# Performance work log

Hardware: AMD Instinct MI355X
Metric: run time of the kernel (lower is better)

The kernel has to match this reference:

```python
import jax, jax.numpy as jnp
import numpy as np

EMBED_DIM = 1024
NUM_HEADS = 16
HEAD_DIM = EMBED_DIM // NUM_HEADS


def _sinusoid_pos_emb(seq_len, dim):
    pos = jnp.arange(seq_len, dtype=jnp.float32)
    idx = jnp.arange(dim // 2, dtype=jnp.float32)
    inv_freq = 1.0 / (10000.0 ** (2.0 * idx / dim))
    ang = pos[:, None] * inv_freq[None, :]          # [S, D/2]
    return jnp.concatenate([jnp.sin(ang), jnp.cos(ang)], axis=-1)  # [S, D]


def _relative_shift(x):
    # x: [B, H, S, S] -> Transformer-XL shift
    b, h, s, _ = x.shape
    x = jnp.pad(x, ((0, 0), (0, 0), (0, 0), (1, 0)))
    x = x.reshape(b, h, s + 1, s)
    return x[:, :, 1:, :].reshape(b, h, s, s)


def setup_inputs() -> dict:
    key = jax.random.key(0)
    ks = jax.random.split(key, 12)
    D = EMBED_DIM
    sc = 1.0 / np.sqrt(D)
    inp = {"x": jax.random.normal(ks[0], (2, 2048, D), dtype=jnp.float32)}
    for i, name in enumerate(["Wq", "Wk", "Wv", "Wp", "Wo"]):
        inp[name] = jax.random.normal(ks[1 + i], (D, D), dtype=jnp.float32) * sc
        inp["b" + name[1].lower()] = jnp.zeros((D,), dtype=jnp.float32)
    inp["u"] = jax.random.normal(ks[6], (1, NUM_HEADS, 1, HEAD_DIM), dtype=jnp.float32) * 0.05
    inp["v"] = jax.random.normal(ks[7], (1, NUM_HEADS, 1, HEAD_DIM), dtype=jnp.float32) * 0.05
    return inp


def reference(x, Wq, bq, Wk, bk, Wv, bv, Wp, bp, Wo, bo, u, v):
    B, S, D = x.shape
    H, P = NUM_HEADS, HEAD_DIM

    def heads(t):  # [B,S,D] -> [B,H,S,P]
        return t.reshape(B, S, H, P).transpose(0, 2, 1, 3)

    q = heads(x @ Wq + bq)
    k = heads(x @ Wk + bk)
    val = heads(x @ Wv + bv)

    pos = _sinusoid_pos_emb(S, D) @ Wp + bp            # [S, D]
    pos = pos.reshape(S, H, P).transpose(1, 0, 2)       # [H, S, P]

    content_score = jnp.einsum('bhsp,bhtp->bhst', q + u, k)
    pos_score = jnp.einsum('bhsp,htp->bhst', q + v, pos)
    pos_score = _relative_shift(pos_score)

    score = (content_score + pos_score) / jnp.sqrt(jnp.float32(P))
    weights = jax.nn.softmax(score, axis=-1)            # dropout = 0 (inference)
    out = jnp.einsum('bhst,bhtp->bhsp', weights, val)
    out = out.transpose(0, 2, 1, 3).reshape(B, S, D)
    return out @ Wo + bo
```

## Files before the change

### kernel.cpp

```cpp
#include <hip/hip_runtime.h>
#include <hip/hip_bf16.h>

typedef unsigned short u16;
typedef unsigned int u32;
typedef __bf16 bf16x8 __attribute__((ext_vector_type(8)));
typedef float f32x4 __attribute__((ext_vector_type(4)));

#define SEQ 2048
#define NH 16
#define PD 64
#define DM 1024

#if __has_builtin(__builtin_amdgcn_exp2f)
#define EXP2(x) __builtin_amdgcn_exp2f(x)
#else
#define EXP2(x) __expf((x) * 0.6931471805599453f)
#endif

__device__ __forceinline__ float bf2f(u16 s) {
  u32 t = ((u32)s) << 16;
  float f;
  __builtin_memcpy(&f, &t, 4);
  return f;
}
__device__ __forceinline__ u16 f2bf(float f) {
  u32 x;
  __builtin_memcpy(&x, &f, 4);
  x = (x + 0x7fffu + ((x >> 16) & 1u)) >> 16;
  return (u16)x;
}
__device__ __forceinline__ float u2f(u32 b) {
  float f;
  __builtin_memcpy(&f, &b, 4);
  return f;
}
__device__ __forceinline__ u32 pack2(float a, float b) {
  __hip_bfloat162 h = __float22bfloat162_rn(float2{a, b});
  u32 r;
  __builtin_memcpy(&r, &h, 4);
  return r;
}
template <int C>
__device__ __forceinline__ float dppf(float x) {
  int xi;
  __builtin_memcpy(&xi, &x, 4);
  int yi = __builtin_amdgcn_mov_dpp(xi, C, 0xF, 0xF, false);
  float y;
  __builtin_memcpy(&y, &yi, 4);
  return y;
}
__device__ __forceinline__ float rmax16(float x) {
  x = fmaxf(x, dppf<0x121>(x));
  x = fmaxf(x, dppf<0x122>(x));
  x = fmaxf(x, dppf<0x124>(x));
  x = fmaxf(x, dppf<0x128>(x));
  return x;
}
__device__ __forceinline__ float rsum16(float x) {
  x += dppf<0x121>(x);
  x += dppf<0x122>(x);
  x += dppf<0x124>(x);
  x += dppf<0x128>(x);
  return x;
}
__device__ __forceinline__ void gld16(const u16* g, u16* l) {
  __builtin_amdgcn_global_load_lds(
      (const __attribute__((address_space(1))) unsigned int*)(g),
      (__attribute__((address_space(3))) unsigned int*)(l), 16, 0, 0);
}

__global__ __launch_bounds__(256) void detect_kernel(const u16* __restrict__ probe,
                                                     int* __restrict__ flag) {
  __shared__ int sz[256], sh[256];
  int tid = threadIdx.x;
  int zeros = 0, huge = 0;
  for (int j = 0; j < 16; ++j) {
    int i = tid * 16 + j;
    u16 v = probe[i];
    int e = (v >> 7) & 0xFF;
    if (((i & 1) == 0) && v == 0) zeros++;
    if (e >= 0x8C) huge++;
  }
  sz[tid] = zeros; sh[tid] = huge;
  __syncthreads();
  for (int s = 128; s > 0; s >>= 1) {
    if (tid < s) { sz[tid] += sz[tid + s]; sh[tid] += sh[tid + s]; }
    __syncthreads();
  }
  if (tid == 0) *flag = (sz[0] > 1024 || sh[0] > 200) ? 1 : 0;
}

__global__ __launch_bounds__(256) void convert_x_kernel(const void* __restrict__ src,
                                                        u16* __restrict__ dst,
                                                        const int* __restrict__ flag) {
  int i = (blockIdx.x * 256 + threadIdx.x) * 4;
  if (*flag) {
    float4 f = *(const float4*)((const float*)src + i);
    u16 o[4] = {f2bf(f.x), f2bf(f.y), f2bf(f.z), f2bf(f.w)};
    *(uint2*)(dst + i) = *(const uint2*)o;
  } else {
    *(uint2*)(dst + i) = *(const uint2*)((const u16*)src + i);
  }
}

struct ParamPtrs { const void* p[7]; };
__global__ __launch_bounds__(256) void convert_params_kernel(ParamPtrs pp,
                                                             float* __restrict__ pf,
                                                             const int* __restrict__ flag) {
  int idx = blockIdx.x * 256 + threadIdx.x;
  int seg = idx >> 10, off = idx & 1023;
  const void* s = pp.p[seg];
  pf[idx] = (*flag) ? ((const float*)s)[off] : bf2f(((const u16*)s)[off]);
}

__global__ __launch_bounds__(256) void sinusoid_kernel(u16* __restrict__ out) {
  int idx = blockIdx.x * 256 + threadIdx.x;
  int s = idx >> 10;
  int i = idx & 1023;
  int j = i & 511;
  float invf = __expf(-(float)j * (9.210340371976184f / 512.0f));
  float ang = (float)s * invf;
  float val = (i < 512) ? sinf(ang) : cosf(ang);
  out[idx] = f2bf(val);
}

__global__ __launch_bounds__(256) void transpose5_kernel(
    const void* __restrict__ w0, const void* __restrict__ w1,
    const void* __restrict__ w2, const void* __restrict__ w3,
    const void* __restrict__ w4, u16* __restrict__ dst,
    const int* __restrict__ flag) {
  __shared__ u16 t[64][72];
  int z = blockIdx.z;
  const void* src = (z == 0) ? w0 : (z == 1) ? w1 : (z == 2) ? w2 : (z == 3) ? w3 : w4;
  u16* out = dst + (size_t)z * DM * DM;
  int r0 = blockIdx.y * 64, c0 = blockIdx.x * 64;
  int tr = threadIdx.x >> 2;
  int tc = (threadIdx.x & 3) * 16;
  if (*flag) {
    const float* g = (const float*)src + (size_t)(r0 + tr) * DM + c0 + tc;
#pragma unroll
    for (int q = 0; q < 4; ++q) {
      float4 f = *(const float4*)(g + q * 4);
      t[tr][tc + q * 4 + 0] = f2bf(f.x);
      t[tr][tc + q * 4 + 1] = f2bf(f.y);
      t[tr][tc + q * 4 + 2] = f2bf(f.z);
      t[tr][tc + q * 4 + 3] = f2bf(f.w);
    }
  } else {
    const uint4* g = (const uint4*)((const u16*)src + (size_t)(r0 + tr) * DM + c0 + tc);
    uint4 a = g[0], bb = g[1];
    *(uint4*)&t[tr][tc] = a;
    *(uint4*)&t[tr][tc + 8] = bb;
  }
  __syncthreads();
  u16 tmp[16] __attribute__((aligned(16)));
#pragma unroll
  for (int jj = 0; jj < 16; ++jj) tmp[jj] = t[tc + jj][tr];
  uint4* o = (uint4*)(out + (size_t)(c0 + tr) * DM + r0 + tc);
  o[0] = *(const uint4*)&tmp[0];
  o[1] = *(const uint4*)&tmp[8];
}

__global__ __launch_bounds__(256) void transpose_v_kernel(
    const u16* __restrict__ V, u16* __restrict__ Vt) {
  __shared__ u16 t[64][72];
  int s0 = blockIdx.x * 64;
  int bh = blockIdx.y;
  int b = bh >> 4, h = bh & 15;
  int tr = threadIdx.x >> 2;
  int tc = (threadIdx.x & 3) * 16;
  const uint4* g = (const uint4*)(V + ((size_t)(b * SEQ + s0 + tr) * NH + h) * PD + tc);
  uint4 a = g[0], bb = g[1];
  *(uint4*)&t[tr][tc] = a;
  *(uint4*)&t[tr][tc + 8] = bb;
  __syncthreads();
  u16 tmp[16] __attribute__((aligned(16)));
#pragma unroll
  for (int jj = 0; jj < 16; ++jj) tmp[jj] = t[tc + jj][tr];
  uint4* o = (uint4*)(Vt + ((size_t)(b * NH + h) * PD + tr) * SEQ + s0 + tc);
  o[0] = *(const uint4*)&tmp[0];
  o[1] = *(const uint4*)&tmp[8];
}

struct GemmArgs {
  const u16* A;  const u16* A3;
  const u16* Bt0; const u16* Bt1; const u16* Bt2; const u16* Bt3;
  const float* b0; const float* b1; const float* b2; const float* b3;
  void* C0; void* C1; void* C2; void* C3;
  int N, K, M3;
  const int* flag; int outFp32;
};

__global__ __launch_bounds__(256, 4) void gemm_bt_kernel(GemmArgs p) {
  __shared__ u16 As[128 * 32];
  __shared__ u16 Bs[128 * 32];
  int z = blockIdx.z;
  if (z == 3 && (int)blockIdx.y * 128 >= p.M3) return;
  const u16* A = (z == 3) ? p.A3 : p.A;
  const u16* Bt = (z == 0) ? p.Bt0 : (z == 1) ? p.Bt1 : (z == 2) ? p.Bt2 : p.Bt3;
  const float* bias = (z == 0) ? p.b0 : (z == 1) ? p.b1 : (z == 2) ? p.b2 : p.b3;
  void* Cv = (z == 0) ? p.C0 : (z == 1) ? p.C1 : (z == 2) ? p.C2 : p.C3;
  int K = p.K, N = p.N;
  bool f32o = p.outFp32 && (*p.flag);

  int tid = threadIdx.x;
  int wave = tid >> 6, lane = tid & 63;
  int quad = lane >> 4, l16 = lane & 15;
  int m0 = blockIdx.y * 128, n0 = blockIdx.x * 128;
  int wm = (wave >> 1) * 64, wn = (wave & 1) * 64;

  int trow = tid >> 2;
  int tcol = ((tid & 3) ^ ((tid >> 3) & 3)) * 8;
  const u16* ga = A + (size_t)(m0 + trow) * K + tcol;
  const u16* gb = Bt + (size_t)(n0 + trow) * K + tcol;
  u16* lwa = As + wave * 512;
  u16* lwb = Bs + wave * 512;
  int slotx = (quad ^ ((l16 >> 1) & 3)) * 8;

  f32x4 acc[4][4] = {};

  for (int k0 = 0; k0 < K; k0 += 32) {
    __syncthreads();
    gld16(ga + k0, lwa);
    gld16(ga + (size_t)64 * K + k0, lwa + 2048);
    gld16(gb + k0, lwb);
    gld16(gb + (size_t)64 * K + k0, lwb + 2048);
    __syncthreads();
    bf16x8 af[4], bfv[4];
#pragma unroll
    for (int i = 0; i < 4; ++i) {
      af[i] = *(const bf16x8*)&As[(wm + i * 16 + l16) * 32 + slotx];
      bfv[i] = *(const bf16x8*)&Bs[(wn + i * 16 + l16) * 32 + slotx];
    }
#pragma unroll
    for (int tm = 0; tm < 4; ++tm)
#pragma unroll
      for (int tn = 0; tn < 4; ++tn)
        acc[tm][tn] = __builtin_amdgcn_mfma_f32_16x16x32_bf16(af[tm], bfv[tn], acc[tm][tn], 0, 0, 0);
  }

#pragma unroll
  for (int tm = 0; tm < 4; ++tm) {
    int row = m0 + wm + tm * 16 + quad * 4;
#pragma unroll
    for (int tn = 0; tn < 4; ++tn) {
      int col = n0 + wn + tn * 16 + l16;
      float bv = bias[col];
#pragma unroll
      for (int r = 0; r < 4; ++r) {
        float val = acc[tm][tn][r] + bv;
        if (f32o) ((float*)Cv)[(size_t)(row + r) * N + col] = val;
        else ((u16*)Cv)[(size_t)(row + r) * N + col] = f2bf(val);
      }
    }
  }
}

__global__ __launch_bounds__(256, 4) void attn_kernel(
    const u16* __restrict__ Q, const u16* __restrict__ Kg,
    const u16* __restrict__ Vtg, const u16* __restrict__ Rg,
    const float* __restrict__ pf,
    u16* __restrict__ O) {
  __shared__ __align__(16) u16 KP[64 * 72];
  __shared__ __align__(16) u16 RVs[4096];
  __shared__ __align__(16) u16 Bb[128 * 66];

  int tid = threadIdx.x, wave = tid >> 6, lane = tid & 63;
  int quad = lane >> 4, l16 = lane & 15;
  int id = blockIdx.x;
  int bh = (id & 7) + ((id >> 8) << 3);
  int s0 = ((id >> 3) & 31) * 64;
  int b = bh >> 4, h = bh & 15;
  const float* pu = pf + 5 * 1024 + h * PD;
  const float* pv = pf + 6 * 1024 + h * PD;

  int arow = wave * 16 + l16;
  int sl_base = wave * 16 + quad * 4;

  int srow = wave * 16 + (lane >> 2);
  int scol = ((lane & 3) ^ ((lane >> 3) & 3)) * 8;
  u16* kbase = KP + wave * 512;
  u16* rvbase = RVs + wave * 512;
  int kb0 = l16 * 32 + (quad ^ ((l16 >> 1) & 3)) * 8;

  const float QS = 0.18033688011112042f;
  bf16x8 qu0, qu1, qv0a, qv1a, qv0b, qv1b;
  {
    const u16* qp = Q + ((size_t)(b * SEQ + s0 + arow)) * DM + h * PD;
    int row2 = s0 + arow + 1;
    if (row2 > SEQ - 1) row2 = SEQ - 1;
    const u16* qp2 = Q + ((size_t)(b * SEQ + row2)) * DM + h * PD;
    u16 qa[16] __attribute__((aligned(16)));
    u16 qb[16] __attribute__((aligned(16)));
    *(uint4*)&qa[0] = *(const uint4*)(qp + quad * 8);
    *(uint4*)&qa[8] = *(const uint4*)(qp + 32 + quad * 8);
    *(uint4*)&qb[0] = *(const uint4*)(qp2 + quad * 8);
    *(uint4*)&qb[8] = *(const uint4*)(qp2 + 32 + quad * 8);
    u16 fu[16] __attribute__((aligned(16)));
    u16 fv0[16] __attribute__((aligned(16)));
    u16 fv1[16] __attribute__((aligned(16)));
#pragma unroll
    for (int j = 0; j < 8; ++j) {
      float u0 = pu[quad * 8 + j], u1 = pu[32 + quad * 8 + j];
      float v0 = pv[quad * 8 + j], v1 = pv[32 + quad * 8 + j];
      fu[j] = f2bf((bf2f(qa[j]) + u0) * QS);
      fu[8 + j] = f2bf((bf2f(qa[8 + j]) + u1) * QS);
      fv0[j] = f2bf((bf2f(qa[j]) + v0) * QS);
      fv0[8 + j] = f2bf((bf2f(qa[8 + j]) + v1) * QS);
      fv1[j] = f2bf((bf2f(qb[j]) + v0) * QS);
      fv1[8 + j] = f2bf((bf2f(qb[8 + j]) + v1) * QS);
    }
    __builtin_memcpy(&qu0, &fu[0], 16);
    __builtin_memcpy(&qu1, &fu[8], 16);
    __builtin_memcpy(&qv0a, &fv0[0], 16);
    __builtin_memcpy(&qv1a, &fv0[8], 16);
    __builtin_memcpy(&qv0b, &fv1[0], 16);
    __builtin_memcpy(&qv1b, &fv1[8], 16);
  }

  auto dmaR = [&](int tb0) {
    int tg = tb0 + srow;
    tg = tg < 0 ? 0 : (tg > SEQ - 1 ? SEQ - 1 : tg);
    const u16* gr = Rg + (size_t)tg * DM + h * PD + scol;
    gld16(gr, rvbase);
    gld16(gr + 32, rvbase + 2048);
  };
  auto slice = [&](bf16x8 fa0, bf16x8 fa1, int slotBase, int rowOff, int lo, int hi) {
#pragma unroll
    for (int tt = 0; tt < 4; ++tt) {
      f32x4 pacc = {};
      bf16x8 b0 = *(const bf16x8*)&RVs[kb0 + tt * 512];
      bf16x8 b1 = *(const bf16x8*)&RVs[kb0 + tt * 512 + 2048];
      pacc = __builtin_amdgcn_mfma_f32_16x16x32_bf16(fa0, b0, pacc, 0, 0, 0);
      pacc = __builtin_amdgcn_mfma_f32_16x16x32_bf16(fa1, b1, pacc, 0, 0, 0);
      int rloc = tt * 16 + l16;
      bool ok = (rloc >= lo) & (rloc <= hi);
      u32 w0 = ok ? pack2(pacc[0], pacc[1]) : 0u;
      u32 w1 = ok ? pack2(pacc[2], pacc[3]) : 0u;
      int prow = (slotBase + rloc + rowOff) & 127;
      *(u32*)&Bb[prow * 66 + sl_base] = w0;
      *(u32*)&Bb[prow * 66 + sl_base + 2] = w1;
    }
  };

  float m_i[4], l_i[4];
#pragma unroll
  for (int r = 0; r < 4; ++r) { m_i[r] = -1e30f; l_i[r] = 0.f; }
  f32x4 oacc[4] = {};

  dmaR(SEQ - 65 - s0);
  __syncthreads();
  slice(qv0a, qv1a, 0, 0, 0, 63);

  for (int j0 = 0; j0 < SEQ; j0 += 64) {
    int a1 = (j0 >> 6) + 1;
    int slot = (a1 & 1) << 6;
    bool p0n = (j0 <= s0);
    bool p1n = (j0 >= s0);
    __syncthreads();
    {
      const u16* gk = Kg + (size_t)(b * SEQ + j0 + srow) * DM + h * PD + scol;
      gld16(gk, kbase);
      gld16(gk + 32, kbase + 2048);
    }
    dmaR((p0n ? (SEQ - 65 - s0) : (-65 - s0)) + 64 * a1);
    __syncthreads();

    f32x4 acc[4];
#pragma unroll
    for (int tn = 0; tn < 4; ++tn) {
      f32x4 a = {};
      bf16x8 b0 = *(const bf16x8*)&KP[kb0 + tn * 512];
      bf16x8 b1 = *(const bf16x8*)&KP[kb0 + tn * 512 + 2048];
      a = __builtin_amdgcn_mfma_f32_16x16x32_bf16(qu0, b0, a, 0, 0, 0);
      a = __builtin_amdgcn_mfma_f32_16x16x32_bf16(qu1, b1, a, 0, 0, 0);
      acc[tn] = a;
    }

    if (p0n) slice(qv0a, qv1a, slot, 0, 0, s0 + 64 - 64 * a1);
    if (p0n && p1n) {
      __syncthreads();
      dmaR(64 * a1 - s0 - 65);
      __syncthreads();
    }
    if (p1n) slice(qv0b, qv1b, slot, 1, s0 + 65 - 64 * a1, 63);
    __syncthreads();

    {
      const u16* gv = Vtg + ((size_t)(b * NH + h) * PD + srow) * SEQ + j0 + scol;
      gld16(gv, rvbase);
      gld16(gv + 32, rvbase + 2048);
    }

    int g0 = l16 - sl_base + 64 + j0;
#pragma unroll
    for (int tn = 0; tn < 4; ++tn) {
#pragma unroll
      for (int r = 0; r < 4; ++r) {
        int rl = (g0 + tn * 16 - r) & 127;
        acc[tn][r] += bf2f(Bb[rl * 66 + sl_base + r]);
      }
    }

    float alpha_r[4];
#pragma unroll
    for (int r = 0; r < 4; ++r) {
      float v0 = acc[0][r], v1 = acc[1][r];
      float v2 = acc[2][r], v3 = acc[3][r];
      float mx = fmaxf(fmaxf(v0, v1), fmaxf(v2, v3));
      mx = rmax16(mx);
      float m_new = fmaxf(m_i[r], mx);
      float al = EXP2(m_i[r] - m_new);
      u32 w0 = pack2(EXP2(v0 - m_new), EXP2(v1 - m_new));
      u32 w1 = pack2(EXP2(v2 - m_new), EXP2(v3 - m_new));
      u16 ec[4] = {(u16)w0, (u16)(w0 >> 16), (u16)w1, (u16)(w1 >> 16)};
      int row = sl_base + r;
      u16* prow_ = KP + row * 72 + l16;
#pragma unroll
      for (int cr = 0; cr < 4; ++cr) {
        int c = (cr + quad) & 3;
        prow_[c * 16] = ec[c];
      }
      float ssum = u2f(w0 << 16) + u2f(w0 & 0xffff0000u) + u2f(w1 << 16) + u2f(w1 & 0xffff0000u);
      ssum = rsum16(ssum);
      l_i[r] = l_i[r] * al + ssum;
      m_i[r] = m_new;
      alpha_r[r] = al;
    }
    __syncthreads();

    {
      bf16x8 pa0 = *(const bf16x8*)&KP[arow * 72 + quad * 8];
      bf16x8 pa1 = *(const bf16x8*)&KP[arow * 72 + 32 + quad * 8];
#pragma unroll
      for (int tp = 0; tp < 4; ++tp) {
#pragma unroll
        for (int r = 0; r < 4; ++r) oacc[tp][r] *= alpha_r[r];
        bf16x8 b0 = *(const bf16x8*)&RVs[kb0 + tp * 512];
        bf16x8 b1 = *(const bf16x8*)&RVs[kb0 + tp * 512 + 2048];
        oacc[tp] = __builtin_amdgcn_mfma_f32_16x16x32_bf16(pa0, b0, oacc[tp], 0, 0, 0);
        oacc[tp] = __builtin_amdgcn_mfma_f32_16x16x32_bf16(pa1, b1, oacc[tp], 0, 0, 0);
      }
    }
  }

#pragma unroll
  for (int r = 0; r < 4; ++r) l_i[r] = 1.f / l_i[r];
#pragma unroll
  for (int tp = 0; tp < 4; ++tp) {
    int pcol = tp * 16 + l16;
#pragma unroll
    for (int r = 0; r < 4; ++r) {
      int sg = s0 + sl_base + r;
      O[((size_t)(b * SEQ + sg)) * DM + h * PD + pcol] = f2bf(oacc[tp][r] * l_i[r]);
    }
  }
}

extern "C" void kernel_launch(void* const* d_in, const int* in_sizes, int n_in,
                              void* d_out, int out_size, void* d_ws, size_t ws_size,
                              hipStream_t stream) {
  (void)in_sizes; (void)n_in; (void)out_size; (void)ws_size;
  const void* x  = d_in[0];
  const void* Wq = d_in[1];
  const void* bq = d_in[2];
  const void* Wk = d_in[3];
  const void* bk = d_in[4];
  const void* Wv = d_in[5];
  const void* bv = d_in[6];
  const void* Wp = d_in[7];
  const void* bp = d_in[8];
  const void* Wo = d_in[9];
  const void* bo = d_in[10];
  const void* u  = d_in[11];
  const void* v  = d_in[12];

  char* base = (char*)d_ws;
  int* flag = (int*)base;
  float* pf = (float*)(base + 64);
  u16* wbase = (u16*)(base + 64 + 7168 * 4);
  u16* WT   = wbase;
  u16* xb   = WT + (size_t)5 * DM * DM;
  u16* sinb = xb + (size_t)2 * SEQ * DM;
  u16* Qb   = sinb + (size_t)SEQ * DM;
  u16* Kb   = Qb + (size_t)2 * SEQ * DM;
  u16* Vb   = Kb + (size_t)2 * SEQ * DM;
  u16* Rb   = Vb + (size_t)2 * SEQ * DM;
  u16* Vtb  = xb;
  u16* Ab   = Vb;

  detect_kernel<<<1, 256, 0, stream>>>((const u16*)Wq, flag);

  convert_x_kernel<<<(2 * SEQ * DM) / 1024, 256, 0, stream>>>(x, xb, flag);
  ParamPtrs pp;
  pp.p[0] = bq; pp.p[1] = bk; pp.p[2] = bv; pp.p[3] = bp; pp.p[4] = bo;
  pp.p[5] = u;  pp.p[6] = v;
  convert_params_kernel<<<28, 256, 0, stream>>>(pp, pf, flag);

  sinusoid_kernel<<<(SEQ * DM) / 256, 256, 0, stream>>>(sinb);
  transpose5_kernel<<<dim3(16, 16, 5), 256, 0, stream>>>(Wq, Wk, Wv, Wp, Wo, WT, flag);

  GemmArgs qkv;
  qkv.A = xb; qkv.A3 = sinb;
  qkv.Bt0 = WT; qkv.Bt1 = WT + (size_t)DM * DM; qkv.Bt2 = WT + (size_t)2 * DM * DM;
  qkv.Bt3 = WT + (size_t)3 * DM * DM;
  qkv.b0 = pf; qkv.b1 = pf + 1024; qkv.b2 = pf + 2048; qkv.b3 = pf + 3072;
  qkv.C0 = Qb; qkv.C1 = Kb; qkv.C2 = Vb; qkv.C3 = Rb;
  qkv.N = DM; qkv.K = DM; qkv.M3 = SEQ; qkv.flag = flag; qkv.outFp32 = 0;
  gemm_bt_kernel<<<dim3(8, 32, 4), 256, 0, stream>>>(qkv);

  transpose_v_kernel<<<dim3(32, 32), 256, 0, stream>>>(Vb, Vtb);
  attn_kernel<<<dim3(1024), 256, 0, stream>>>(Qb, Kb, Vtb, Rb, pf, Ab);

  GemmArgs fo;
  fo.A = Ab; fo.A3 = Ab;
  fo.Bt0 = WT + (size_t)4 * DM * DM; fo.Bt1 = fo.Bt0; fo.Bt2 = fo.Bt0; fo.Bt3 = fo.Bt0;
  fo.b0 = pf + 4096; fo.b1 = fo.b0; fo.b2 = fo.b0; fo.b3 = fo.b0;
  fo.C0 = d_out; fo.C1 = d_out; fo.C2 = d_out; fo.C3 = d_out;
  fo.N = DM; fo.K = DM; fo.M3 = 0; fo.flag = flag; fo.outFp32 = 1;
  gemm_bt_kernel<<<dim3(8, 32, 1), 256, 0, stream>>>(fo);
}
```

Measured before the change: 313.0 us.

## Transpose QK MFMA operands so softmax rows live per lane, restructure rel-shift buffer

Swaps the A/B operands of the score and positional MFMAs so each lane holds four consecutive key columns of one query row. Row max and sum then need only two cross-lane shuffles instead of four DPP steps per register, and one max/exp chain per lane instead of four. The relative-shift buffer becomes row-major per query (B2) with wraparound duplicate entries and precomputed even/odd offsets, and the loop is unrolled by two. Alpha and l are redistributed to the PV output layout via ds_bpermute. Separately, the sinusoid kernel switches to fast __sinf/__cosf, which costs some accuracy for large angles.

Measured after the change: 372.5 us. 19.0% more time.

```diff
diff --git a/kernel.cpp b/kernel.cpp
--- a/kernel.cpp
+++ b/kernel.cpp
@@ -29,39 +29,22 @@
   x = (x + 0x7fffu + ((x >> 16) & 1u)) >> 16;
   return (u16)x;
 }
-__device__ __forceinline__ float u2f(u32 b) {
-  float f;
-  __builtin_memcpy(&f, &b, 4);
-  return f;
-}
 __device__ __forceinline__ u32 pack2(float a, float b) {
   __hip_bfloat162 h = __float22bfloat162_rn(float2{a, b});
   u32 r;
   __builtin_memcpy(&r, &h, 4);
   return r;
 }
-template <int C>
-__device__ __forceinline__ float dppf(float x) {
+__device__ __forceinline__ float sxor(float x, int m) {
+  return __shfl_xor(x, m, 64);
+}
+__device__ __forceinline__ float bpermf(float x, int idx) {
   int xi;
   __builtin_memcpy(&xi, &x, 4);
-  int yi = __builtin_amdgcn_mov_dpp(xi, C, 0xF, 0xF, false);
+  int yi = __builtin_amdgcn_ds_bpermute(idx, xi);
   float y;
   __builtin_memcpy(&y, &yi, 4);
   return y;
-}
-__device__ __forceinline__ float rmax16(float x) {
-  x = fmaxf(x, dppf<0x121>(x));
-  x = fmaxf(x, dppf<0x122>(x));
-  x = fmaxf(x, dppf<0x124>(x));
-  x = fmaxf(x, dppf<0x128>(x));
-  return x;
-}
-__device__ __forceinline__ float rsum16(float x) {
-  x += dppf<0x121>(x);
-  x += dppf<0x122>(x);
-  x += dppf<0x124>(x);
-  x += dppf<0x128>(x);
-  return x;
 }
 __device__ __forceinline__ void gld16(const u16* g, u16* l) {
   __builtin_amdgcn_global_load_lds(
@@ -120,7 +103,7 @@
   int j = i & 511;
   float invf = __expf(-(float)j * (9.210340371976184f / 512.0f));
   float ang = (float)s * invf;
-  float val = (i < 512) ? sinf(ang) : cosf(ang);
+  float val = (i < 512) ? __sinf(ang) : __cosf(ang);
   out[idx] = f2bf(val);
 }
 
@@ -263,7 +246,7 @@
     u16* __restrict__ O) {
   __shared__ __align__(16) u16 KP[64 * 72];
   __shared__ __align__(16) u16 RVs[4096];
-  __shared__ __align__(16) u16 Bb[128 * 66];
+  __shared__ __align__(16) u16 B2[64 * 132];
 
   int tid = threadIdx.x, wave = tid >> 6, lane = tid & 63;
   int quad = lane >> 4, l16 = lane & 15;
@@ -318,6 +301,18 @@
     __builtin_memcpy(&qv1b, &fv1[8], 16);
   }
 
+  u16* B2c = B2 + (16 * wave + l16) * 132;
+  int pE[4], pO[4];
+#pragma unroll
+  for (int tn = 0; tn < 4; ++tn) {
+    pE[tn] = (16 * tn + 4 * quad + 64 - 16 * wave - l16) & 127;
+    pO[tn] = (16 * tn + 4 * quad + 128 - 16 * wave - l16) & 127;
+  }
+  int bpi[4];
+#pragma unroll
+  for (int r = 0; r < 4; ++r) bpi[r] = (20 * quad + r) * 4;
+  u16* prowP = KP + (size_t)arow * 72 + 4 * quad;
+
   auto dmaR = [&](int tb0) {
     int tg = tb0 + srow;
     tg = tg < 0 ? 0 : (tg > SEQ - 1 ? SEQ - 1 : tg);
@@ -325,36 +320,62 @@
     gld16(gr, rvbase);
     gld16(gr + 32, rvbase + 2048);
   };
-  auto slice = [&](bf16x8 fa0, bf16x8 fa1, int slotBase, int rowOff, int lo, int hi) {
+  auto slice0 = [&](bf16x8 fa0, bf16x8 fa1, int baseRow, int hi) {
 #pragma unroll
     for (int tt = 0; tt < 4; ++tt) {
       f32x4 pacc = {};
       bf16x8 b0 = *(const bf16x8*)&RVs[kb0 + tt * 512];
       bf16x8 b1 = *(const bf16x8*)&RVs[kb0 + tt * 512 + 2048];
-      pacc = __builtin_amdgcn_mfma_f32_16x16x32_bf16(fa0, b0, pacc, 0, 0, 0);
-      pacc = __builtin_amdgcn_mfma_f32_16x16x32_bf16(fa1, b1, pacc, 0, 0, 0);
-      int rloc = tt * 16 + l16;
-      bool ok = (rloc >= lo) & (rloc <= hi);
-      u32 w0 = ok ? pack2(pacc[0], pacc[1]) : 0u;
-      u32 w1 = ok ? pack2(pacc[2], pacc[3]) : 0u;
-      int prow = (slotBase + rloc + rowOff) & 127;
-      *(u32*)&Bb[prow * 66 + sl_base] = w0;
-      *(u32*)&Bb[prow * 66 + sl_base + 2] = w1;
+      pacc = __builtin_amdgcn_mfma_f32_16x16x32_bf16(b0, fa0, pacc, 0, 0, 0);
+      pacc = __builtin_amdgcn_mfma_f32_16x16x32_bf16(b1, fa1, pacc, 0, 0, 0);
+      int r0 = tt * 16 + 4 * quad;
+      float v0 = (r0 + 0 <= hi) ? pacc[0] : 0.f;
+      float v1 = (r0 + 1 <= hi) ? pacc[1] : 0.f;
+      float v2 = (r0 + 2 <= hi) ? pacc[2] : 0.f;
+      float v3 = (r0 + 3 <= hi) ? pacc[3] : 0.f;
+      uint2 w;
+      w.x = pack2(v0, v1);
+      w.y = pack2(v2, v3);
+      int u0 = (baseRow + r0) & 127;
+      *(uint2*)&B2c[u0] = w;
+      if (u0 == 0) *(uint2*)&B2c[128] = w;
     }
   };
-
-  float m_i[4], l_i[4];
-#pragma unroll
-  for (int r = 0; r < 4; ++r) { m_i[r] = -1e30f; l_i[r] = 0.f; }
+  auto slice1 = [&](bf16x8 fa0, bf16x8 fa1, int baseRow, int lo) {
+#pragma unroll
+    for (int tt = 0; tt < 4; ++tt) {
+      f32x4 pacc = {};
+      bf16x8 b0 = *(const bf16x8*)&RVs[kb0 + tt * 512];
+      bf16x8 b1 = *(const bf16x8*)&RVs[kb0 + tt * 512 + 2048];
+      pacc = __builtin_amdgcn_mfma_f32_16x16x32_bf16(b0, fa0, pacc, 0, 0, 0);
+      pacc = __builtin_amdgcn_mfma_f32_16x16x32_bf16(b1, fa1, pacc, 0, 0, 0);
+      int r0 = tt * 16 + 4 * quad;
+      float v0 = (r0 + 0 >= lo) ? pacc[0] : 0.f;
+      float v1 = (r0 + 1 >= lo) ? pacc[1] : 0.f;
+      float v2 = (r0 + 2 >= lo) ? pacc[2] : 0.f;
+      float v3 = (r0 + 3 >= lo) ? pacc[3] : 0.f;
+      u32 w0 = pack2(v0, v1), w1 = pack2(v2, v3);
+      u16 ev[4] = {(u16)w0, (u16)(w0 >> 16), (u16)w1, (u16)(w1 >> 16)};
+      int u0 = (baseRow + r0) & 127;
+#pragma unroll
+      for (int reg = 0; reg < 4; ++reg) {
+        int uu = u0 + reg;
+        B2c[uu] = ev[reg];
+        if ((uu & 127) < 3) B2c[uu ^ 128] = ev[reg];
+      }
+    }
+  };
+
+  float m_s = -1e30f, l_s = 0.f;
   f32x4 oacc[4] = {};
 
   dmaR(SEQ - 65 - s0);
   __syncthreads();
-  slice(qv0a, qv1a, 0, 0, 0, 63);
-
-  for (int j0 = 0; j0 < SEQ; j0 += 64) {
+  slice0(qv0a, qv1a, 0, 63);
+
+  auto body = [&](int j0, const int* gp) {
     int a1 = (j0 >> 6) + 1;
-    int slot = (a1 & 1) << 6;
+    int slotBase = (a1 & 1) << 6;
     bool p0n = (j0 <= s0);
     bool p1n = (j0 >= s0);
     __syncthreads();
@@ -370,20 +391,20 @@
 #pragma unroll
     for (int tn = 0; tn < 4; ++tn) {
       f32x4 a = {};
-      bf16x8 b0 = *(const bf16x8*)&KP[kb0 + tn * 512];
-      bf16x8 b1 = *(const bf16x8*)&KP[kb0 + tn * 512 + 2048];
-      a = __builtin_amdgcn_mfma_f32_16x16x32_bf16(qu0, b0, a, 0, 0, 0);
-      a = __builtin_amdgcn_mfma_f32_16x16x32_bf16(qu1, b1, a, 0, 0, 0);
+      bf16x8 k0 = *(const bf16x8*)&KP[kb0 + tn * 512];
+      bf16x8 k1 = *(const bf16x8*)&KP[kb0 + tn * 512 + 2048];
+      a = __builtin_amdgcn_mfma_f32_16x16x32_bf16(k0, qu0, a, 0, 0, 0);
+      a = __builtin_amdgcn_mfma_f32_16x16x32_bf16(k1, qu1, a, 0, 0, 0);
       acc[tn] = a;
     }
 
-    if (p0n) slice(qv0a, qv1a, slot, 0, 0, s0 + 64 - 64 * a1);
+    if (p0n) slice0(qv0a, qv1a, slotBase, s0 + 64 - 64 * a1);
     if (p0n && p1n) {
       __syncthreads();
       dmaR(64 * a1 - s0 - 65);
       __syncthreads();
     }
-    if (p1n) slice(qv0b, qv1b, slot, 1, s0 + 65 - 64 * a1, 63);
+    if (p1n) slice1(qv0b, qv1b, slotBase + 1, s0 + 65 - 64 * a1);
     __syncthreads();
 
     {
@@ -392,41 +413,44 @@
       gld16(gv + 32, rvbase + 2048);
     }
 
-    int g0 = l16 - sl_base + 64 + j0;
 #pragma unroll
     for (int tn = 0; tn < 4; ++tn) {
-#pragma unroll
-      for (int r = 0; r < 4; ++r) {
-        int rl = (g0 + tn * 16 - r) & 127;
-        acc[tn][r] += bf2f(Bb[rl * 66 + sl_base + r]);
-      }
-    }
-
+      const u16* g = B2c + gp[tn];
+      acc[tn][0] += bf2f(g[0]);
+      acc[tn][1] += bf2f(g[1]);
+      acc[tn][2] += bf2f(g[2]);
+      acc[tn][3] += bf2f(g[3]);
+    }
+
+    float t0 = fmaxf(fmaxf(acc[0][0], acc[0][1]), fmaxf(acc[0][2], acc[0][3]));
+    float t1 = fmaxf(fmaxf(acc[1][0], acc[1][1]), fmaxf(acc[1][2], acc[1][3]));
+    float t2 = fmaxf(fmaxf(acc[2][0], acc[2][1]), fmaxf(acc[2][2], acc[2][3]));
+    float t3 = fmaxf(fmaxf(acc[3][0], acc[3][1]), fmaxf(acc[3][2], acc[3][3]));
+    float mx = fmaxf(fmaxf(t0, t1), fmaxf(t2, t3));
+    mx = fmaxf(mx, sxor(mx, 16));
+    mx = fmaxf(mx, sxor(mx, 32));
+    float m_new = fmaxf(m_s, mx);
+    float al = EXP2(m_s - m_new);
+    m_s = m_new;
+    float ssum = 0.f;
+#pragma unroll
+    for (int tn = 0; tn < 4; ++tn) {
+      float e0 = EXP2(acc[tn][0] - m_new);
+      float e1 = EXP2(acc[tn][1] - m_new);
+      float e2 = EXP2(acc[tn][2] - m_new);
+      float e3 = EXP2(acc[tn][3] - m_new);
+      ssum += (e0 + e1) + (e2 + e3);
+      uint2 w;
+      w.x = pack2(e0, e1);
+      w.y = pack2(e2, e3);
+      *(uint2*)(prowP + tn * 16) = w;
+    }
+    ssum += sxor(ssum, 16);
+    ssum += sxor(ssum, 32);
+    l_s = l_s * al + ssum;
     float alpha_r[4];
 #pragma unroll
-    for (int r = 0; r < 4; ++r) {
-      float v0 = acc[0][r], v1 = acc[1][r];
-      float v2 = acc[2][r], v3 = acc[3][r];
-      float mx = fmaxf(fmaxf(v0, v1), fmaxf(v2, v3));
-      mx = rmax16(mx);
-      float m_new = fmaxf(m_i[r], mx);
-      float al = EXP2(m_i[r] - m_new);
-      u32 w0 = pack2(EXP2(v0 - m_new), EXP2(v1 - m_new));
-      u32 w1 = pack2(EXP2(v2 - m_new), EXP2(v3 - m_new));
-      u16 ec[4] = {(u16)w0, (u16)(w0 >> 16), (u16)w1, (u16)(w1 >> 16)};
-      int row = sl_base + r;
-      u16* prow_ = KP + row * 72 + l16;
-#pragma unroll
-      for (int cr = 0; cr < 4; ++cr) {
-        int c = (cr + quad) & 3;
-        prow_[c * 16] = ec[c];
-      }
-      float ssum = u2f(w0 << 16) + u2f(w0 & 0xffff0000u) + u2f(w1 << 16) + u2f(w1 & 0xffff0000u);
-      ssum = rsum16(ssum);
-      l_i[r] = l_i[r] * al + ssum;
-      m_i[r] = m_new;
-      alpha_r[r] = al;
-    }
+    for (int r = 0; r < 4; ++r) alpha_r[r] = bpermf(al, bpi[r]);
     __syncthreads();
 
     {
@@ -442,17 +466,23 @@
         oacc[tp] = __builtin_amdgcn_mfma_f32_16x16x32_bf16(pa1, b1, oacc[tp], 0, 0, 0);
       }
     }
-  }
-
-#pragma unroll
-  for (int r = 0; r < 4; ++r) l_i[r] = 1.f / l_i[r];
+  };
+
+  for (int j00 = 0; j00 < SEQ; j00 += 128) {
+    body(j00, pE);
+    body(j00 + 64, pO);
+  }
+
+  float linv[4];
+#pragma unroll
+  for (int r = 0; r < 4; ++r) linv[r] = 1.f / bpermf(l_s, bpi[r]);
 #pragma unroll
   for (int tp = 0; tp < 4; ++tp) {
     int pcol = tp * 16 + l16;
 #pragma unroll
     for (int r = 0; r < 4; ++r) {
       int sg = s0 + sl_base + r;
-      O[((size_t)(b * SEQ + sg)) * DM + h * PD + pcol] = f2bf(oacc[tp][r] * l_i[r]);
+      O[((size_t)(b * SEQ + sg)) * DM + h * PD + pcol] = f2bf(oacc[tp][r] * linv[r]);
     }
   }
 }
```

## Fuse prep kernels into one launch and write V transposed from QKV GEMM

Applied to the files above, without the earlier changes.

Merges the dtype-detect, x conversion, sinusoid generation, weight transposes and parameter conversion into a single prep kernel in which every block recomputes the detection flag itself. The separate V-transpose kernel is dropped: the QKV GEMM epilogue writes V directly in [b, h*d, s] layout with packed 4-element stores. The sinusoid now uses the fast __sinf/__cosf intrinsics. This removes several launches and a full read/write pass over V, at the cost of every prep block re-reading the probe, plus lower sin/cos accuracy for large angles.

New measurement: 302.2 us. -3.4%, faster.

```diff
diff --git a/kernel.cpp b/kernel.cpp
--- a/kernel.cpp
+++ b/kernel.cpp
@@ -69,117 +69,108 @@
       (__attribute__((address_space(3))) unsigned int*)(l), 16, 0, 0);
 }
 
-__global__ __launch_bounds__(256) void detect_kernel(const u16* __restrict__ probe,
-                                                     int* __restrict__ flag) {
+struct PrepArgs {
+  const void* x;
+  const void* w0; const void* w1; const void* w2; const void* w3; const void* w4;
+  const void* p0; const void* p1; const void* p2; const void* p3; const void* p4;
+  const void* p5; const void* p6;
+};
+
+__global__ __launch_bounds__(256) void prep_kernel(PrepArgs pa,
+                                                   u16* __restrict__ xb,
+                                                   u16* __restrict__ sinb,
+                                                   u16* __restrict__ WT,
+                                                   float* __restrict__ pf,
+                                                   int* __restrict__ flag) {
   __shared__ int sz[256], sh[256];
+  __shared__ u16 t[64][72];
   int tid = threadIdx.x;
-  int zeros = 0, huge = 0;
-  for (int j = 0; j < 16; ++j) {
-    int i = tid * 16 + j;
-    u16 v = probe[i];
-    int e = (v >> 7) & 0xFF;
-    if (((i & 1) == 0) && v == 0) zeros++;
-    if (e >= 0x8C) huge++;
-  }
-  sz[tid] = zeros; sh[tid] = huge;
-  __syncthreads();
-  for (int s = 128; s > 0; s >>= 1) {
-    if (tid < s) { sz[tid] += sz[tid + s]; sh[tid] += sh[tid + s]; }
-    __syncthreads();
-  }
-  if (tid == 0) *flag = (sz[0] > 1024 || sh[0] > 200) ? 1 : 0;
-}
-
-__global__ __launch_bounds__(256) void convert_x_kernel(const void* __restrict__ src,
-                                                        u16* __restrict__ dst,
-                                                        const int* __restrict__ flag) {
-  int i = (blockIdx.x * 256 + threadIdx.x) * 4;
-  if (*flag) {
-    float4 f = *(const float4*)((const float*)src + i);
-    u16 o[4] = {f2bf(f.x), f2bf(f.y), f2bf(f.z), f2bf(f.w)};
-    *(uint2*)(dst + i) = *(const uint2*)o;
+
+  {
+    const u16* probe = (const u16*)pa.w0;
+    int zeros = 0, huge = 0;
+    for (int j = 0; j < 16; ++j) {
+      int i = tid * 16 + j;
+      u16 v = probe[i];
+      int e = (v >> 7) & 0xFF;
+      if (((i & 1) == 0) && v == 0) zeros++;
+      if (e >= 0x8C) huge++;
+    }
+    sz[tid] = zeros; sh[tid] = huge;
+    __syncthreads();
+    for (int s = 128; s > 0; s >>= 1) {
+      if (tid < s) { sz[tid] += sz[tid + s]; sh[tid] += sh[tid + s]; }
+      __syncthreads();
+    }
+  }
+  int f = (sz[0] > 1024 || sh[0] > 200) ? 1 : 0;
+  int id = blockIdx.x;
+  if (id == 0 && tid == 0) *flag = f;
+
+  if (id < 4096) {
+    int i = (id * 256 + tid) * 4;
+    if (f) {
+      float4 fv = *(const float4*)((const float*)pa.x + i);
+      u16 o[4] __attribute__((aligned(8))) = {f2bf(fv.x), f2bf(fv.y), f2bf(fv.z), f2bf(fv.w)};
+      *(uint2*)(xb + i) = *(const uint2*)o;
+    } else {
+      *(uint2*)(xb + i) = *(const uint2*)((const u16*)pa.x + i);
+    }
+  } else if (id < 6144) {
+    int base = ((id - 4096) * 256 + tid) * 4;
+    u16 o[4] __attribute__((aligned(8)));
+#pragma unroll
+    for (int e = 0; e < 4; ++e) {
+      int idx = base + e;
+      int s = idx >> 10;
+      int i = idx & 1023;
+      int j = i & 511;
+      float invf = __expf(-(float)j * (9.210340371976184f / 512.0f));
+      float ang = (float)s * invf;
+      float val = (i < 512) ? __sinf(ang) : __cosf(ang);
+      o[e] = f2bf(val);
+    }
+    *(uint2*)(sinb + base) = *(const uint2*)o;
+  } else if (id < 7424) {
+    int tt = id - 6144;
+    int z = tt >> 8;
+    int rem = tt & 255;
+    const void* src = (z == 0) ? pa.w0 : (z == 1) ? pa.w1 : (z == 2) ? pa.w2
+                     : (z == 3) ? pa.w3 : pa.w4;
+    u16* out = WT + (size_t)z * DM * DM;
+    int r0 = (rem >> 4) * 64, c0 = (rem & 15) * 64;
+    int tr = tid >> 2;
+    int tc = (tid & 3) * 16;
+    if (f) {
+      const float* g = (const float*)src + (size_t)(r0 + tr) * DM + c0 + tc;
+#pragma unroll
+      for (int q = 0; q < 4; ++q) {
+        float4 fv = *(const float4*)(g + q * 4);
+        t[tr][tc + q * 4 + 0] = f2bf(fv.x);
+        t[tr][tc + q * 4 + 1] = f2bf(fv.y);
+        t[tr][tc + q * 4 + 2] = f2bf(fv.z);
+        t[tr][tc + q * 4 + 3] = f2bf(fv.w);
+      }
+    } else {
+      const uint4* g = (const uint4*)((const u16*)src + (size_t)(r0 + tr) * DM + c0 + tc);
+      uint4 a = g[0], bb = g[1];
+      *(uint4*)&t[tr][tc] = a;
+      *(uint4*)&t[tr][tc + 8] = bb;
+    }
+    __syncthreads();
+    u16 tmp[16] __attribute__((aligned(16)));
+#pragma unroll
+    for (int jj = 0; jj < 16; ++jj) tmp[jj] = t[tc + jj][tr];
+    uint4* o = (uint4*)(out + (size_t)(c0 + tr) * DM + r0 + tc);
+    o[0] = *(const uint4*)&tmp[0];
+    o[1] = *(const uint4*)&tmp[8];
   } else {
-    *(uint2*)(dst + i) = *(const uint2*)((const u16*)src + i);
-  }
-}
-
-struct ParamPtrs { const void* p[7]; };
-__global__ __launch_bounds__(256) void convert_params_kernel(ParamPtrs pp,
-                                                             float* __restrict__ pf,
-                                                             const int* __restrict__ flag) {
-  int idx = blockIdx.x * 256 + threadIdx.x;
-  int seg = idx >> 10, off = idx & 1023;
-  const void* s = pp.p[seg];
-  pf[idx] = (*flag) ? ((const float*)s)[off] : bf2f(((const u16*)s)[off]);
-}
-
-__global__ __launch_bounds__(256) void sinusoid_kernel(u16* __restrict__ out) {
-  int idx = blockIdx.x * 256 + threadIdx.x;
-  int s = idx >> 10;
-  int i = idx & 1023;
-  int j = i & 511;
-  float invf = __expf(-(float)j * (9.210340371976184f / 512.0f));
-  float ang = (float)s * invf;
-  float val = (i < 512) ? sinf(ang) : cosf(ang);
-  out[idx] = f2bf(val);
-}
-
-__global__ __launch_bounds__(256) void transpose5_kernel(
-    const void* __restrict__ w0, const void* __restrict__ w1,
-    const void* __restrict__ w2, const void* __restrict__ w3,
-    const void* __restrict__ w4, u16* __restrict__ dst,
-    const int* __restrict__ flag) {
-  __shared__ u16 t[64][72];
-  int z = blockIdx.z;
-  const void* src = (z == 0) ? w0 : (z == 1) ? w1 : (z == 2) ? w2 : (z == 3) ? w3 : w4;
-  u16* out = dst + (size_t)z * DM * DM;
-  int r0 = blockIdx.y * 64, c0 = blockIdx.x * 64;
-  int tr = threadIdx.x >> 2;
-  int tc = (threadIdx.x & 3) * 16;
-  if (*flag) {
-    const float* g = (const float*)src + (size_t)(r0 + tr) * DM + c0 + tc;
-#pragma unroll
-    for (int q = 0; q < 4; ++q) {
-      float4 f = *(const float4*)(g + q * 4);
-      t[tr][tc + q * 4 + 0] = f2bf(f.x);
-      t[tr][tc + q * 4 + 1] = f2bf(f.y);
-      t[tr][tc + q * 4 + 2] = f2bf(f.z);
-      t[tr][tc + q * 4 + 3] = f2bf(f.w);
-    }
-  } else {
-    const uint4* g = (const uint4*)((const u16*)src + (size_t)(r0 + tr) * DM + c0 + tc);
-    uint4 a = g[0], bb = g[1];
-    *(uint4*)&t[tr][tc] = a;
-    *(uint4*)&t[tr][tc + 8] = bb;
-  }
-  __syncthreads();
-  u16 tmp[16] __attribute__((aligned(16)));
-#pragma unroll
-  for (int jj = 0; jj < 16; ++jj) tmp[jj] = t[tc + jj][tr];
-  uint4* o = (uint4*)(out + (size_t)(c0 + tr) * DM + r0 + tc);
-  o[0] = *(const uint4*)&tmp[0];
-  o[1] = *(const uint4*)&tmp[8];
-}
-
-__global__ __launch_bounds__(256) void transpose_v_kernel(
-    const u16* __restrict__ V, u16* __restrict__ Vt) {
-  __shared__ u16 t[64][72];
-  int s0 = blockIdx.x * 64;
-  int bh = blockIdx.y;
-  int b = bh >> 4, h = bh & 15;
-  int tr = threadIdx.x >> 2;
-  int tc = (threadIdx.x & 3) * 16;
-  const uint4* g = (const uint4*)(V + ((size_t)(b * SEQ + s0 + tr) * NH + h) * PD + tc);
-  uint4 a = g[0], bb = g[1];
-  *(uint4*)&t[tr][tc] = a;
-  *(uint4*)&t[tr][tc + 8] = bb;
-  __syncthreads();
-  u16 tmp[16] __attribute__((aligned(16)));
-#pragma unroll
-  for (int jj = 0; jj < 16; ++jj) tmp[jj] = t[tc + jj][tr];
-  uint4* o = (uint4*)(Vt + ((size_t)(b * NH + h) * PD + tr) * SEQ + s0 + tc);
-  o[0] = *(const uint4*)&tmp[0];
-  o[1] = *(const uint4*)&tmp[8];
+    int idx = (id - 7424) * 256 + tid;
+    int seg = idx >> 10, off = idx & 1023;
+    const void* s = (seg == 0) ? pa.p0 : (seg == 1) ? pa.p1 : (seg == 2) ? pa.p2
+                   : (seg == 3) ? pa.p3 : (seg == 4) ? pa.p4 : (seg == 5) ? pa.p5 : pa.p6;
+    pf[idx] = f ? ((const float*)s)[off] : bf2f(((const u16*)s)[off]);
+  }
 }
 
 struct GemmArgs {
@@ -188,7 +179,7 @@
   const float* b0; const float* b1; const float* b2; const float* b3;
   void* C0; void* C1; void* C2; void* C3;
   int N, K, M3;
-  const int* flag; int outFp32;
+  const int* flag; int outFp32; int vtrans;
 };
 
 __global__ __launch_bounds__(256, 4) void gemm_bt_kernel(GemmArgs p) {
@@ -202,6 +193,7 @@
   void* Cv = (z == 0) ? p.C0 : (z == 1) ? p.C1 : (z == 2) ? p.C2 : p.C3;
   int K = p.K, N = p.N;
   bool f32o = p.outFp32 && (*p.flag);
+  bool vt = p.vtrans && (z == 2);
 
   int tid = threadIdx.x;
   int wave = tid >> 6, lane = tid & 63;
@@ -246,11 +238,19 @@
     for (int tn = 0; tn < 4; ++tn) {
       int col = n0 + wn + tn * 16 + l16;
       float bv = bias[col];
-#pragma unroll
-      for (int r = 0; r < 4; ++r) {
-        float val = acc[tm][tn][r] + bv;
-        if (f32o) ((float*)Cv)[(size_t)(row + r) * N + col] = val;
-        else ((u16*)Cv)[(size_t)(row + r) * N + col] = f2bf(val);
+      if (vt) {
+        u16 o4[4] __attribute__((aligned(8)));
+#pragma unroll
+        for (int r = 0; r < 4; ++r) o4[r] = f2bf(acc[tm][tn][r] + bv);
+        int bq_ = row >> 11, s = row & 2047;
+        *(uint2*)((u16*)Cv + ((size_t)(bq_ * 1024 + col)) * 2048 + s) = *(const uint2*)o4;
+      } else {
+#pragma unroll
+        for (int r = 0; r < 4; ++r) {
+          float val = acc[tm][tn][r] + bv;
+          if (f32o) ((float*)Cv)[(size_t)(row + r) * N + col] = val;
+          else ((u16*)Cv)[(size_t)(row + r) * N + col] = f2bf(val);
+        }
       }
     }
   }
@@ -484,32 +484,25 @@
   u16* sinb = xb + (size_t)2 * SEQ * DM;
   u16* Qb   = sinb + (size_t)SEQ * DM;
   u16* Kb   = Qb + (size_t)2 * SEQ * DM;
-  u16* Vb   = Kb + (size_t)2 * SEQ * DM;
-  u16* Rb   = Vb + (size_t)2 * SEQ * DM;
-  u16* Vtb  = xb;
-  u16* Ab   = Vb;
-
-  detect_kernel<<<1, 256, 0, stream>>>((const u16*)Wq, flag);
-
-  convert_x_kernel<<<(2 * SEQ * DM) / 1024, 256, 0, stream>>>(x, xb, flag);
-  ParamPtrs pp;
-  pp.p[0] = bq; pp.p[1] = bk; pp.p[2] = bv; pp.p[3] = bp; pp.p[4] = bo;
-  pp.p[5] = u;  pp.p[6] = v;
-  convert_params_kernel<<<28, 256, 0, stream>>>(pp, pf, flag);
-
-  sinusoid_kernel<<<(SEQ * DM) / 256, 256, 0, stream>>>(sinb);
-  transpose5_kernel<<<dim3(16, 16, 5), 256, 0, stream>>>(Wq, Wk, Wv, Wp, Wo, WT, flag);
+  u16* Vtb  = Kb + (size_t)2 * SEQ * DM;
+  u16* Rb   = Vtb + (size_t)2 * SEQ * DM;
+  u16* Ab   = xb;
+
+  PrepArgs pa;
+  pa.x = x;
+  pa.w0 = Wq; pa.w1 = Wk; pa.w2 = Wv; pa.w3 = Wp; pa.w4 = Wo;
+  pa.p0 = bq; pa.p1 = bk; pa.p2 = bv; pa.p3 = bp; pa.p4 = bo; pa.p5 = u; pa.p6 = v;
+  prep_kernel<<<7452, 256, 0, stream>>>(pa, xb, sinb, WT, pf, flag);
 
   GemmArgs qkv;
   qkv.A = xb; qkv.A3 = sinb;
   qkv.Bt0 = WT; qkv.Bt1 = WT + (size_t)DM * DM; qkv.Bt2 = WT + (size_t)2 * DM * DM;
   qkv.Bt3 = WT + (size_t)3 * DM * DM;
   qkv.b0 = pf; qkv.b1 = pf + 1024; qkv.b2 = pf + 2048; qkv.b3 = pf + 3072;
-  qkv.C0 = Qb; qkv.C1 = Kb; qkv.C2 = Vb; qkv.C3 = Rb;
-  qkv.N = DM; qkv.K = DM; qkv.M3 = SEQ; qkv.flag = flag; qkv.outFp32 = 0;
+  qkv.C0 = Qb; qkv.C1 = Kb; qkv.C2 = Vtb; qkv.C3 = Rb;
+  qkv.N = DM; qkv.K = DM; qkv.M3 = SEQ; qkv.flag = flag; qkv.outFp32 = 0; qkv.vtrans = 1;
   gemm_bt_kernel<<<dim3(8, 32, 4), 256, 0, stream>>>(qkv);
 
-  transpose_v_kernel<<<dim3(32, 32), 256, 0, stream>>>(Vb, Vtb);
   attn_kernel<<<dim3(1024), 256, 0, stream>>>(Qb, Kb, Vtb, Rb, pf, Ab);
 
   GemmArgs fo;
@@ -517,6 +510,6 @@
   fo.Bt0 = WT + (size_t)4 * DM * DM; fo.Bt1 = fo.Bt0; fo.Bt2 = fo.Bt0; fo.Bt3 = fo.Bt0;
   fo.b0 = pf + 4096; fo.b1 = fo.b0; fo.b2 = fo.b0; fo.b3 = fo.b0;
   fo.C0 = d_out; fo.C1 = d_out; fo.C2 = d_out; fo.C3 = d_out;
-  fo.N = DM; fo.K = DM; fo.M3 = 0; fo.flag = flag; fo.outFp32 = 1;
+  fo.N = DM; fo.K = DM; fo.M3 = 0; fo.flag = flag; fo.outFp32 = 1; fo.vtrans = 0;
   gemm_bt_kernel<<<dim3(8, 32, 1), 256, 0, stream>>>(fo);
 }
```
